# Optimization experiments

Hardware: AMD Instinct MI355X
Metric: run time of the kernel (lower is better)

The kernel has to match this reference:

```python
import math
import jax, jax.numpy as jnp
import numpy as np

L_MAX = 3
PADDED = (1, 1, 2, 3)            # padded_l_list
K_MAX_L = (128, 96, 64, 32)      # channel bounds per l
FEATS = (32, 32, 32, 32)         # k_max_l[l] - k_max_l[l+1]
N_ATOMS = 20000
N_EDGES = 80000
N_RADIAL = 32
HIDDEN = 128
EPS = 1e-6


def setup_inputs() -> dict:
    key = jax.random.key(0)
    ks = jax.random.split(key, 40)
    it = iter(range(40))
    nk = lambda: ks[next(it)]
    inp = {}
    inp['rb'] = jax.random.normal(nk(), (L_MAX + 1, N_EDGES, N_RADIAL), jnp.float32)
    for l in range(L_MAX + 1):
        inp[f'sh{l}'] = jax.random.normal(nk(), (N_EDGES, 2 * l + 1), jnp.float32)
    for l in range(L_MAX + 1):
        P = PADDED[l]
        inp[f'f{l}'] = jax.random.normal(nk(), (N_ATOMS, P + 1, P + 1, FEATS[l]), jnp.float32)
    for P in (1, 2, 3):
        n = (P + 1) ** 2
        inp[f'U{P}'] = jax.random.normal(nk(), (n, n), jnp.float32) / math.sqrt(n)
    inp['gammas'] = jnp.ones((L_MAX + 1, 32), jnp.float32)
    inp['Win'] = jax.random.normal(nk(), (L_MAX + 1, 32, 32), jnp.float32) / math.sqrt(32.0)
    inp['Wout'] = jax.random.normal(nk(), (L_MAX + 1, 32, 32), jnp.float32) / math.sqrt(32.0)
    inp['A'] = jax.random.normal(nk(), (L_MAX + 1, N_RADIAL, HIDDEN), jnp.float32) / math.sqrt(float(N_RADIAL))
    for l in range(L_MAX + 1):
        inp[f'B{l}'] = jax.random.normal(nk(), (HIDDEN, K_MAX_L[l]), jnp.float32) / math.sqrt(float(HIDDEN))
    inp['msg_scale'] = jnp.float32(0.5)
    inp['centers'] = jax.random.randint(nk(), (N_EDGES,), 0, N_ATOMS)
    inp['neighbors'] = jax.random.randint(nk(), (N_EDGES,), 0, N_ATOMS)
    return inp


def _forward(rb, shs, feats, Us, gammas, Win, Wout, A, Bs, msg_scale, centers, neighbors):
    n_atoms = feats[0].shape[0]
    # EquivariantRMSNorm (norm over uncoupled i,j indices per channel) + linear_in
    h = []
    for l in range(L_MAX + 1):
        f = feats[l]
        rms = jnp.sqrt(jnp.mean(f * f, axis=(1, 2), keepdims=True) + EPS)
        fn = (f / rms) * gammas[l]
        h.append(jnp.einsum('nijf,fg->nijg', fn, Win[l]))
    # per-l radial MLP: [E, n_radial] -> silu -> [E, k_max_l[l]]
    rbm = [jax.nn.silu(rb[l] @ A[l]) @ Bs[l] for l in range(L_MAX + 1)]
    # vector expansion [E, 2l+1, k_max_l[l]]
    vexp = [shs[l][:, :, None] * rbm[l][:, None, :] for l in range(L_MAX + 1)]
    # split channels into per-l groups, uncouple via CG matrix U
    unc = []
    for l in range(L_MAX + 1):
        lower = K_MAX_L[l + 1] if l < L_MAX else 0
        upper = K_MAX_L[l]
        group = [vexp[lp][:, :, lower:upper] for lp in range(l + 1)]
        P = PADDED[l]
        if len(group) < P + 1:
            group.append(jnp.zeros((N_EDGES, 2 * P + 1, upper - lower), group[0].dtype))
        stacked = jnp.concatenate(group, axis=1)  # [E, (P+1)^2, feat]
        u = jnp.einsum('pq,eqf->epf', Us[P], stacked)
        unc.append(u.reshape(N_EDGES, P + 1, P + 1, upper - lower))
    # gather -> per-l tensor product -> scatter-add -> linear_out -> residual
    out = []
    for l in range(L_MAX + 1):
        P = PADDED[l]
        msg = jnp.einsum('eijf,ejkf->eikf', unc[l], h[l][neighbors]) / math.sqrt(P + 1.0)
        pooled = jnp.zeros((n_atoms,) + msg.shape[1:], msg.dtype).at[centers].add(msg) * msg_scale
        out.append(feats[l] + jnp.einsum('nijf,fg->nijg', pooled, Wout[l]))
    return tuple(out)


def reference(rb, sh0, sh1, sh2, sh3, f0, f1, f2, f3, U1, U2, U3, gammas, Win, Wout, A, B0, B1, B2, B3, msg_scale, centers, neighbors):
    return _forward(rb, [sh0, sh1, sh2, sh3], [f0, f1, f2, f3], {1: U1, 2: U2, 3: U3}, gammas, Win, Wout, A, [B0, B1, B2, B3], msg_scale, centers, neighbors)
```

## Files before the change

### kernel.cpp

```cpp
#include <hip/hip_runtime.h>
#include <cstdint>

#define NA 20000
#define NE 80000

typedef __attribute__((ext_vector_type(8))) short short8;
typedef __attribute__((ext_vector_type(4))) float f32x4;
typedef unsigned short ushort_t;

constexpr int HOFFc[4]   = {0, 2560000, 5120000, 10880000};
constexpr int RBMOFFc[4] = {0, 128, 224, 288};

__device__ __forceinline__ ushort_t f2bf(float x) {
    union { float f; unsigned u; } v; v.f = x;
    unsigned r = v.u + 0x7fffu + ((v.u >> 16) & 1u);
    return (ushort_t)(r >> 16);
}
__device__ __forceinline__ float bf2f(ushort_t u) {
    union { unsigned u; float f; } v; v.u = ((unsigned)u) << 16;
    return v.f;
}
__device__ __forceinline__ unsigned pack2(float a, float b) {
    return ((unsigned)f2bf(b) << 16) | (unsigned)f2bf(a);
}

__global__ __launch_bounds__(256)
void k_prep_w(const float* __restrict__ B0, const float* __restrict__ B1,
              const float* __restrict__ B2, const float* __restrict__ B3,
              const float* __restrict__ A, const float* __restrict__ Win,
              ushort_t* __restrict__ BT, ushort_t* __restrict__ ATb,
              ushort_t* __restrict__ WinTb)
{
    const int i = blockIdx.x * 256 + threadIdx.x;
    if (i < 40960) {
        const int n = i >> 7, k = i & 127;
        const float* src; int nl, N;
        if (n < 128)      { src = B0; nl = n;       N = 128; }
        else if (n < 224) { src = B1; nl = n - 128; N = 96;  }
        else if (n < 288) { src = B2; nl = n - 224; N = 64;  }
        else              { src = B3; nl = n - 288; N = 32;  }
        BT[i] = f2bf(src[k * N + nl]);
    } else if (i < 57344) {
        const int j2 = i - 40960;
        const int l = j2 >> 12, rem = j2 & 4095, jrow = rem >> 5, k = rem & 31;
        ATb[j2] = f2bf(A[l * 4096 + k * 128 + jrow]);
    } else if (i < 61440) {
        const int j3 = i - 57344;
        const int l = j3 >> 10, rem = j3 & 1023, g = rem >> 5, k = rem & 31;
        WinTb[j3] = f2bf(Win[l * 1024 + k * 32 + g]);
    }
}

template<int S, int AB>
__device__ __forceinline__ void norm_body(
    const float* __restrict__ fsel, const float* __restrict__ gammas, int l,
    const ushort_t* __restrict__ WinTb, ushort_t* __restrict__ hb,
    ushort_t* __restrict__ s_wt, float* __restrict__ s_scale)
{
    const int t = threadIdx.x;
    const int na0 = blockIdx.x * AB;

    if (t < 128) {
        reinterpret_cast<uint4*>(s_wt)[t] =
            reinterpret_cast<const uint4*>(WinTb + l * 1024)[t];
    }
    for (int i = t; i < AB * 32; i += 256) {
        const int a = i >> 5, c = i & 31;
        int aa = na0 + a; if (aa > NA - 1) aa = NA - 1;
        const float* fp = fsel + ((size_t)aa * S) * 32 + c;
        float ss = 0.f;
        #pragma unroll
        for (int s = 0; s < S; ++s) { const float v = fp[s * 32]; ss += v * v; }
        s_scale[i] = gammas[l * 32 + c] * rsqrtf(ss / (float)S + 1e-6f);
    }
    __syncthreads();

    const int w = t >> 6, lane = t & 63, l15 = lane & 15, lg = lane >> 4;
    const int row = w * 16 + l15;
    const bool rvalid = row < AB * S;
    const int rowc = rvalid ? row : 0;
    const int a = rowc / S, s = rowc % S;
    const int atom = na0 + a;
    const bool store_ok = rvalid && (atom < NA);
    const int atomc = (atom < NA) ? atom : (NA - 1);

    const float* fp = fsel + ((size_t)atomc * S + s) * 32 + lg * 8;
    const float4 x0 = *reinterpret_cast<const float4*>(fp);
    const float4 x1 = *reinterpret_cast<const float4*>(fp + 4);
    const float4 c0 = *reinterpret_cast<const float4*>(&s_scale[a * 32 + lg * 8]);
    const float4 c1 = *reinterpret_cast<const float4*>(&s_scale[a * 32 + lg * 8 + 4]);

    union { short8 v; unsigned u[4]; } bf;
    bf.u[0] = pack2(x0.x * c0.x, x0.y * c0.y);
    bf.u[1] = pack2(x0.z * c0.z, x0.w * c0.w);
    bf.u[2] = pack2(x1.x * c1.x, x1.y * c1.y);
    bf.u[3] = pack2(x1.z * c1.z, x1.w * c1.w);

    const short8 a0 = *reinterpret_cast<const short8*>(&s_wt[l15 * 32 + lg * 8]);
    const short8 a1 = *reinterpret_cast<const short8*>(&s_wt[(16 + l15) * 32 + lg * 8]);
    f32x4 d0 = __builtin_amdgcn_mfma_f32_16x16x32_bf16(a0, bf.v, (f32x4){0.f,0.f,0.f,0.f}, 0, 0, 0);
    f32x4 d1 = __builtin_amdgcn_mfma_f32_16x16x32_bf16(a1, bf.v, (f32x4){0.f,0.f,0.f,0.f}, 0, 0, 0);

    if (store_ok) {
        ushort_t* hp = hb + ((size_t)atomc * S + s) * 32;
        uint2 o0; o0.x = pack2(d0[0], d0[1]); o0.y = pack2(d0[2], d0[3]);
        uint2 o1; o1.x = pack2(d1[0], d1[1]); o1.y = pack2(d1[2], d1[3]);
        *reinterpret_cast<uint2*>(&hp[0  + 4 * lg]) = o0;
        *reinterpret_cast<uint2*>(&hp[16 + 4 * lg]) = o1;
    }
}

__global__ __launch_bounds__(256, 8)
void k_norm_mfma(const float* __restrict__ f0, const float* __restrict__ f1,
                 const float* __restrict__ f2, const float* __restrict__ f3,
                 const float* __restrict__ gammas, const ushort_t* __restrict__ WinTb,
                 ushort_t* __restrict__ h)
{
    __shared__ ushort_t s_wt[1024];
    __shared__ float s_scale[512];
    const int l = blockIdx.y;
    if (l == 0) {
        if (blockIdx.x >= 1250) return;
        norm_body<4, 16>(f0, gammas, 0, WinTb, h + HOFFc[0], s_wt, s_scale);
    } else if (l == 1) {
        if (blockIdx.x >= 1250) return;
        norm_body<4, 16>(f1, gammas, 1, WinTb, h + HOFFc[1], s_wt, s_scale);
    } else if (l == 2) {
        if (blockIdx.x >= 2858) return;
        norm_body<9, 7>(f2, gammas, 2, WinTb, h + HOFFc[2], s_wt, s_scale);
    } else {
        norm_body<16, 4>(f3, gammas, 3, WinTb, h + HOFFc[3], s_wt, s_scale);
    }
}

__global__ __launch_bounds__(256, 3)
void k_edgeA(const float* __restrict__ rb,
             const float* __restrict__ sh0, const float* __restrict__ sh1,
             const float* __restrict__ sh2, const float* __restrict__ sh3,
             const ushort_t* __restrict__ BT, const ushort_t* __restrict__ ATb,
             ushort_t* __restrict__ rbm, float* __restrict__ shq)
{
    __shared__ ushort_t s_h[8192];
    __shared__ ushort_t s_r2[16384];
    ushort_t* s_rbbf = s_r2;
    ushort_t* s_at   = s_r2 + 2048;
    ushort_t* s_bt   = s_r2;

    const int t  = threadIdx.x;
    const int e0 = blockIdx.x * 64;
    const int l  = blockIdx.y;
    const int w  = t >> 6, lane = t & 63;
    const int l15 = lane & 15, lg = lane >> 4;

    if (l == 0) {
        for (int i = t; i < 1024; i += 256) {
            const int q = i & 15, ge = e0 + (i >> 4);
            float v;
            if (q == 0)      v = sh0[ge];
            else if (q < 4)  v = sh1[ge * 3 + (q - 1)];
            else if (q < 9)  v = sh2[ge * 5 + (q - 4)];
            else             v = sh3[ge * 7 + (q - 9)];
            shq[(size_t)e0 * 16 + i] = v;
        }
    }

    const int Kl[4] = {128, 96, 64, 32};
    const int erow = w * 16 + l15;

    for (int i = t; i < 1024; i += 256) {
        const float2 v = *reinterpret_cast<const float2*>(
            &rb[(size_t)l * NE * 32 + (size_t)e0 * 32 + 2 * i]);
        *reinterpret_cast<unsigned*>(&s_rbbf[2 * i]) = pack2(v.x, v.y);
    }
    {
        const uint4* src = reinterpret_cast<const uint4*>(ATb + (size_t)l * 4096);
        for (int i = t; i < 512; i += 256) reinterpret_cast<uint4*>(s_at)[i] = src[i];
    }
    __syncthreads();

    const short8 rbf = *reinterpret_cast<const short8*>(&s_rbbf[erow * 32 + lg * 8]);
    #pragma unroll
    for (int jt = 0; jt < 8; ++jt) {
        const short8 af = *reinterpret_cast<const short8*>(&s_at[(jt * 16 + l15) * 32 + lg * 8]);
        f32x4 d = __builtin_amdgcn_mfma_f32_16x16x32_bf16(af, rbf, (f32x4){0.f,0.f,0.f,0.f}, 0, 0, 0);
        float s0 = d[0] / (1.f + __expf(-d[0]));
        float s1 = d[1] / (1.f + __expf(-d[1]));
        float s2 = d[2] / (1.f + __expf(-d[2]));
        float s3 = d[3] / (1.f + __expf(-d[3]));
        const int chunk = jt * 2 + (lg >> 1);
        const int base = erow * 128 + ((chunk ^ (erow & 7)) << 3) + (lg & 1) * 4;
        uint2 ov; ov.x = pack2(s0, s1); ov.y = pack2(s2, s3);
        *reinterpret_cast<uint2*>(&s_h[base]) = ov;
    }
    __syncthreads();

    const int K = Kl[l];
    for (int cch = t; cch < (K << 4); cch += 256) {
        const int n = cch >> 4, loc = cch & 15;
        const uint4 v = *reinterpret_cast<const uint4*>(&BT[(size_t)(RBMOFFc[l] + n) * 128 + loc * 8]);
        *reinterpret_cast<uint4*>(&s_bt[n * 128 + ((loc ^ (n & 7)) << 3)]) = v;
    }
    __syncthreads();

    const short8 hf0 = *reinterpret_cast<const short8*>(&s_h[erow * 128 + (((0 + lg) ^ (erow & 7)) << 3)]);
    const short8 hf1 = *reinterpret_cast<const short8*>(&s_h[erow * 128 + (((4 + lg) ^ (erow & 7)) << 3)]);
    const short8 hf2 = *reinterpret_cast<const short8*>(&s_h[erow * 128 + (((8 + lg) ^ (erow & 7)) << 3)]);
    const short8 hf3 = *reinterpret_cast<const short8*>(&s_h[erow * 128 + (((12 + lg) ^ (erow & 7)) << 3)]);

    const int ntn = K >> 4;
    for (int nt = 0; nt < ntn; ++nt) {
        const int n = nt * 16 + l15;
        f32x4 acc = {0.f, 0.f, 0.f, 0.f};
        #pragma unroll
        for (int ks = 0; ks < 4; ++ks) {
            const short8 af = *reinterpret_cast<const short8*>(
                &s_bt[n * 128 + (((ks * 4 + lg) ^ (n & 7)) << 3)]);
            const short8 hfk = (ks == 0) ? hf0 : (ks == 1) ? hf1 : (ks == 2) ? hf2 : hf3;
            acc = __builtin_amdgcn_mfma_f32_16x16x32_bf16(af, hfk, acc, 0, 0, 0);
        }
        uint2 ov;
        ov.x = pack2(acc[0], acc[1]);
        ov.y = pack2(acc[2], acc[3]);
        *reinterpret_cast<uint2*>(&rbm[(size_t)(e0 + erow) * 320 + RBMOFFc[l] + nt * 16 + 4 * lg]) = ov;
    }
}

__global__ __launch_bounds__(256)
void k_hist(const int* __restrict__ centers, int* __restrict__ counts)
{
    const int e = blockIdx.x * 256 + threadIdx.x;
    if (e < NE) atomicAdd(&counts[centers[e]], 1);
}

__global__ __launch_bounds__(1024)
void k_scan(const int* __restrict__ counts, int* __restrict__ offsets)
{
    __shared__ int s_sum[1024];
    const int t = threadIdx.x;
    const int CH = 20;
    const int base = t * CH;
    int n = NA - base; n = n < 0 ? 0 : (n > CH ? CH : n);

    int tot = 0;
    for (int i = 0; i < n; i++) tot += counts[base + i];
    s_sum[t] = tot;
    __syncthreads();
    for (int off = 1; off < 1024; off <<= 1) {
        int v = (t >= off) ? s_sum[t - off] : 0;
        __syncthreads();
        s_sum[t] += v;
        __syncthreads();
    }
    int run = s_sum[t] - tot;
    for (int i = 0; i < n; i++) { offsets[base + i] = run; run += counts[base + i]; }
    if (t == 0) offsets[NA] = NE;
}

__global__ __launch_bounds__(256)
void k_fill(const int* __restrict__ centers, const int* __restrict__ offsets,
            int* __restrict__ cursor, int* __restrict__ elist)
{
    const int e = blockIdx.x * 256 + threadIdx.x;
    if (e < NE) {
        const int ctr = centers[e];
        const int pos = offsets[ctr] + atomicAdd(&cursor[ctr], 1);
        elist[pos] = e;
    }
}

template<int P1, int ASTART, int ACNT>
__device__ __forceinline__ void tp_step(float* __restrict__ acc,
                                        const float* __restrict__ lg,
                                        const ushort_t* __restrict__ lh,
                                        const float* __restrict__ rv, int c)
{
    float un[ACNT];
    #pragma unroll
    for (int pi = 0; pi < ACNT; ++pi) {
        const int p = ASTART + pi;
        float a = 0.f;
        #pragma unroll
        for (int lp = 0; lp < P1; ++lp) a += lg[p * 4 + lp] * rv[lp];
        un[pi] = a;
    }
    #pragma unroll
    for (int ii = 0; ii < ACNT / P1; ++ii) {
        #pragma unroll
        for (int k = 0; k < P1; ++k) {
            float m = 0.f;
            #pragma unroll
            for (int j = 0; j < P1; ++j) m += un[ii * P1 + j] * bf2f(lh[(j * P1 + k) * 32 + c]);
            acc[ii * P1 + k] += m;
        }
    }
}

template<int P1, int LOWER>
__global__ __launch_bounds__(256, 6)
void k_pool_big(const float* __restrict__ Up, float uscale,
                const float* __restrict__ WoutL, const float* __restrict__ msp,
                const float* __restrict__ shq, const ushort_t* __restrict__ rbm,
                const ushort_t* __restrict__ hL, const float* __restrict__ fL,
                float* __restrict__ outL,
                const int* __restrict__ offsets, const int* __restrict__ elist,
                const int* __restrict__ neighbors)
{
    constexpr int S       = P1 * P1;
    constexpr int ACNT0   = (P1 == 4) ? 8 : 6;
    constexpr int ACNT1   = (P1 == 4) ? 8 : 3;
    constexpr int ASTART1 = ACNT0;
    constexpr int NV      = (S * 32) / 8;

    __shared__ float    s_U[S * S];
    __shared__ float    s_w[1024];
    __shared__ ushort_t s_hbuf[4][2][S * 32];
    __shared__ float    s_gbuf[4][2][64];

    const int t = threadIdx.x;
    for (int i = t; i < S * S; i += 256) s_U[i] = Up[i] * uscale;
    for (int i = t; i < 1024; i += 256) s_w[i] = WoutL[i];
    __syncthreads();

    const int w = t >> 6, lane = t & 63, c = lane & 31, half = lane >> 5;
    const int n = blockIdx.x * 4 + w;
    const float ms = *msp;
    const int beg = offsets[n], end = offsets[n + 1];

    const int gp = lane >> 2, glp = lane & 3;
    const int qlo = (glp == 0) ? 0 : (glp == 1) ? 1 : (glp == 2) ? 4 : 9;
    const int qhi = (glp == 0) ? 1 : (glp == 1) ? 4 : (glp == 2) ? 9 : 16;
    const bool gvalid = (gp < S) && (glp < P1);

    float acc[ACNT0];
    #pragma unroll
    for (int x = 0; x < ACNT0; ++x) acc[x] = 0.f;

    ushort_t* lhA = s_hbuf[w][0];
    ushort_t* lhB = s_hbuf[w][1];
    float*    lgA = s_gbuf[w][0];
    float*    lgB = s_gbuf[w][1];

    for (int slot = beg; slot < end; slot += 2) {
        const bool haveB = (slot + 1) < end;
        const int eA = elist[slot];
        const int eB = elist[haveB ? slot + 1 : slot];
        const int nbrA = neighbors[eA];
        const int nbrB = neighbors[eB];

        uint4 vA = {}, vB = {};
        const uint4* hpA = reinterpret_cast<const uint4*>(hL + (size_t)nbrA * (S * 32));
        const uint4* hpB = reinterpret_cast<const uint4*>(hL + (size_t)nbrB * (S * 32));
        if (lane < NV) { vA = hpA[lane]; vB = hpB[lane]; }

        const ushort_t* rrA = rbm + (size_t)eA * 320 + LOWER + c;
        const ushort_t* rrB = rbm + (size_t)eB * 320 + LOWER + c;
        float rvA[4], rvB[4];
        #pragma unroll
        for (int lp = 0; lp < P1; ++lp) { rvA[lp] = bf2f(rrA[RBMOFFc[lp]]); rvB[lp] = bf2f(rrB[RBMOFFc[lp]]); }

        const float* sqA = shq + (size_t)eA * 16;
        const float* sqB = shq + (size_t)eB * 16;
        float gA = 0.f, gB = 0.f;
        if (gvalid) {
            for (int q = qlo; q < qhi; ++q) {
                const float u = s_U[gp * S + q];
                gA += u * sqA[q];
                gB += u * sqB[q];
            }
        }

        if (lane < NV) {
            reinterpret_cast<uint4*>(lhA)[lane] = vA;
            reinterpret_cast<uint4*>(lhB)[lane] = vB;
        }
        lgA[lane] = gA;
        lgB[lane] = gB;

        asm volatile("s_waitcnt lgkmcnt(0)" ::: "memory");

        if (half == 0) tp_step<P1, 0,       ACNT0>(acc, lgA, lhA, rvA, c);
        else           tp_step<P1, ASTART1, ACNT1>(acc, lgA, lhA, rvA, c);
        if (haveB) {
            if (half == 0) tp_step<P1, 0,       ACNT0>(acc, lgB, lhB, rvB, c);
            else           tp_step<P1, ASTART1, ACNT1>(acc, lgB, lhB, rvB, c);
        }
    }

    float* accStage = reinterpret_cast<float*>(s_hbuf[w]);
    if (half == 0) {
        #pragma unroll
        for (int x = 0; x < ACNT0; ++x) accStage[x * 32 + c] = acc[x];
    } else {
        #pragma unroll
        for (int x = 0; x < ACNT1; ++x) accStage[(ASTART1 + x) * 32 + c] = acc[x];
    }
    asm volatile("s_waitcnt lgkmcnt(0)" ::: "memory");

    const float* fp = fL + (size_t)n * (S * 32);
    float* op = outL + (size_t)n * (S * 32);
    for (int s = half; s < S; s += 2) {
        float o = 0.f;
        #pragma unroll
        for (int f = 0; f < 32; f++) o += accStage[s * 32 + f] * s_w[f * 32 + c];
        op[s * 32 + c] = fp[s * 32 + c] + ms * o;
    }
}

__global__ __launch_bounds__(256, 4)
void k_pool_01(const float* __restrict__ U1, const float* __restrict__ Wout,
               const float* __restrict__ msp, const float* __restrict__ shq,
               const ushort_t* __restrict__ rbm, const ushort_t* __restrict__ h,
               const float* __restrict__ f0, const float* __restrict__ f1,
               float* __restrict__ out,
               const int* __restrict__ offsets, const int* __restrict__ elist,
               const int* __restrict__ neighbors)
{
    __shared__ float s_U[16];
    __shared__ float s_w[2048];
    __shared__ float s_acc[4][2][128];

    const int t = threadIdx.x;
    if (t < 16) s_U[t] = U1[t] * 0.70710678118654752f;
    for (int i = t; i < 2048; i += 256) s_w[i] = Wout[i];
    __syncthreads();

    const int w = t >> 6, lane = t & 63, c = lane & 31, half = lane >> 5;
    const int n = blockIdx.x * 4 + w;
    const float ms = *msp;
    const int beg = offsets[n], end = offsets[n + 1];
    const ushort_t* h0 = h;
    const ushort_t* h1 = h + 2560000;

    float acc0[4] = {0.f, 0.f, 0.f, 0.f};
    float acc1[4] = {0.f, 0.f, 0.f, 0.f};

    const int nit = (end - beg + 1) >> 1;
    for (int it = 0; it < nit; ++it) {
        const int slot = beg + it * 2 + half;
        const bool valid = slot < end;
        const int e   = elist[valid ? slot : beg];
        const int nbr = neighbors[e];
        const float fac = valid ? 1.f : 0.f;

        const ushort_t* rrow = rbm + (size_t)e * 320;
        const float rv0  = fac * bf2f(rrow[96 + c]);
        const float rv1a = fac * bf2f(rrow[64 + c]);
        const float rv1b = fac * bf2f(rrow[192 + c]);
        const float* sqp = shq + (size_t)e * 16;
        const float sq0 = sqp[0], sq1 = sqp[1], sq2 = sqp[2], sq3 = sqp[3];

        float hn0[4], hn1[4];
        const ushort_t* hp0 = h0 + (size_t)nbr * 128 + c;
        const ushort_t* hp1 = h1 + (size_t)nbr * 128 + c;
        #pragma unroll
        for (int p = 0; p < 4; ++p) { hn0[p] = bf2f(hp0[p * 32]); hn1[p] = bf2f(hp1[p * 32]); }

        const float st0 = sq0 * rv0;
        float st1[4];
        st1[0] = sq0 * rv1a; st1[1] = sq1 * rv1b; st1[2] = sq2 * rv1b; st1[3] = sq3 * rv1b;

        float unc0[4], unc1[4];
        #pragma unroll
        for (int p = 0; p < 4; ++p) {
            unc0[p] = s_U[p * 4] * st0;
            float a = 0.f;
            #pragma unroll
            for (int q = 0; q < 4; ++q) a += s_U[p * 4 + q] * st1[q];
            unc1[p] = a;
        }
        #pragma unroll
        for (int i = 0; i < 2; ++i) {
            #pragma unroll
            for (int k = 0; k < 2; ++k) {
                float m0 = 0.f, m1 = 0.f;
                #pragma unroll
                for (int j = 0; j < 2; ++j) {
                    m0 += unc0[i * 2 + j] * hn0[j * 2 + k];
                    m1 += unc1[i * 2 + j] * hn1[j * 2 + k];
                }
                acc0[i * 2 + k] += m0;
                acc1[i * 2 + k] += m1;
            }
        }
    }

    #pragma unroll
    for (int s = 0; s < 4; s++) { acc0[s] += __shfl_xor(acc0[s], 32); acc1[s] += __shfl_xor(acc1[s], 32); }
    #pragma unroll
    for (int s = 0; s < 4; s++) if ((s & 1) == half) {
        s_acc[w][0][s * 32 + c] = acc0[s];
        s_acc[w][1][s * 32 + c] = acc1[s];
    }
    __syncthreads();

    const float* fp0 = f0 + (size_t)n * 128;
    const float* fp1 = f1 + (size_t)n * 128;
    float* op0 = out + (size_t)n * 128;
    float* op1 = out + 2560000 + (size_t)n * 128;
    for (int s = half; s < 4; s += 2) {
        float o0 = 0.f, o1 = 0.f;
        #pragma unroll
        for (int f = 0; f < 32; f++) {
            o0 += s_acc[w][0][s * 32 + f] * s_w[f * 32 + c];
            o1 += s_acc[w][1][s * 32 + f] * s_w[1024 + f * 32 + c];
        }
        op0[s * 32 + c] = fp0[s * 32 + c] + ms * o0;
        op1[s * 32 + c] = fp1[s * 32 + c] + ms * o1;
    }
}

extern "C" void kernel_launch(void* const* d_in, const int* in_sizes, int n_in,
                              void* d_out, int out_size, void* d_ws, size_t ws_size,
                              hipStream_t stream)
{
    (void)in_sizes; (void)n_in; (void)out_size;

    const float* rb     = (const float*)d_in[0];
    const float* sh0    = (const float*)d_in[1];
    const float* sh1    = (const float*)d_in[2];
    const float* sh2    = (const float*)d_in[3];
    const float* sh3    = (const float*)d_in[4];
    const float* f0     = (const float*)d_in[5];
    const float* f1     = (const float*)d_in[6];
    const float* f2     = (const float*)d_in[7];
    const float* f3     = (const float*)d_in[8];
    const float* U1     = (const float*)d_in[9];
    const float* U2     = (const float*)d_in[10];
    const float* U3     = (const float*)d_in[11];
    const float* gammas = (const float*)d_in[12];
    const float* Win    = (const float*)d_in[13];
    const float* Wout   = (const float*)d_in[14];
    const float* A      = (const float*)d_in[15];
    const float* B0     = (const float*)d_in[16];
    const float* B1     = (const float*)d_in[17];
    const float* B2     = (const float*)d_in[18];
    const float* B3     = (const float*)d_in[19];
    const float* msp    = (const float*)d_in[20];
    const int* centers   = (const int*)d_in[21];
    const int* neighbors = (const int*)d_in[22];

    const size_t OFF_RBM = 42240000;
    const size_t OFF_SHQ = 93440000;
    const size_t OFF_BT  = 98560000;
    const size_t OFF_AT  = 98641920;
    const size_t OFF_WT  = 98674688;
    const size_t OFF_INT = 98682880;
    const size_t needed  = OFF_INT + (size_t)140001 * 4;
    if (ws_size < needed) return;

    ushort_t* h_bf  = (ushort_t*)d_ws;
    ushort_t* rbm   = (ushort_t*)((char*)d_ws + OFF_RBM);
    float*    shq   = (float*)((char*)d_ws + OFF_SHQ);
    ushort_t* BT    = (ushort_t*)((char*)d_ws + OFF_BT);
    ushort_t* ATb   = (ushort_t*)((char*)d_ws + OFF_AT);
    ushort_t* WinTb = (ushort_t*)((char*)d_ws + OFF_WT);
    int* ibase   = (int*)((char*)d_ws + OFF_INT);
    int* offsets = ibase;
    int* counts  = ibase + 20001;
    int* cursor  = ibase + 40001;
    int* elist   = ibase + 60001;

    hipMemsetAsync(counts, 0, (size_t)40000 * sizeof(int), stream);

    k_hist<<<313, 256, 0, stream>>>(centers, counts);
    k_scan<<<1, 1024, 0, stream>>>(counts, offsets);
    k_fill<<<313, 256, 0, stream>>>(centers, offsets, cursor, elist);
    k_prep_w<<<240, 256, 0, stream>>>(B0, B1, B2, B3, A, Win, BT, ATb, WinTb);

    dim3 gN(5000, 4);
    k_norm_mfma<<<gN, 256, 0, stream>>>(f0, f1, f2, f3, gammas, WinTb, h_bf);
    dim3 gE(1250, 4);
    k_edgeA<<<gE, 256, 0, stream>>>(rb, sh0, sh1, sh2, sh3, BT, ATb, rbm, shq);

    float* out = (float*)d_out;
    k_pool_01<<<5000, 256, 0, stream>>>(U1, Wout, msp, shq, rbm, h_bf, f0, f1, out,
                                        offsets, elist, neighbors);
    k_pool_big<3, 32><<<5000, 256, 0, stream>>>(U2, 0.57735026918962576f, Wout + 2048, msp,
                                                shq, rbm, h_bf + HOFFc[2], f2, out + HOFFc[2],
                                                offsets, elist, neighbors);
    k_pool_big<4, 0><<<5000, 256, 0, stream>>>(U3, 0.5f, Wout + 3072, msp,
                                               shq, rbm, h_bf + HOFFc[3], f3, out + HOFFc[3],
                                               offsets, elist, neighbors);
}
```

Baseline: 306.8 us.

## Merge three pooling kernels into one launch and fuse histogram with weight prep

```diff
diff --git a/kernel.cpp b/kernel.cpp
--- a/kernel.cpp
+++ b/kernel.cpp
@@ -25,13 +25,20 @@
 }
 
 __global__ __launch_bounds__(256)
-void k_prep_w(const float* __restrict__ B0, const float* __restrict__ B1,
-              const float* __restrict__ B2, const float* __restrict__ B3,
-              const float* __restrict__ A, const float* __restrict__ Win,
-              ushort_t* __restrict__ BT, ushort_t* __restrict__ ATb,
-              ushort_t* __restrict__ WinTb)
-{
-    const int i = blockIdx.x * 256 + threadIdx.x;
+void k_hist_prep(const int* __restrict__ centers, int* __restrict__ counts,
+                 const float* __restrict__ B0, const float* __restrict__ B1,
+                 const float* __restrict__ B2, const float* __restrict__ B3,
+                 const float* __restrict__ A, const float* __restrict__ Win,
+                 ushort_t* __restrict__ BT, ushort_t* __restrict__ ATb,
+                 ushort_t* __restrict__ WinTb)
+{
+    const int b = blockIdx.x;
+    if (b < 313) {
+        const int e = b * 256 + threadIdx.x;
+        if (e < NE) atomicAdd(&counts[centers[e]], 1);
+        return;
+    }
+    const int i = (b - 313) * 256 + threadIdx.x;
     if (i < 40960) {
         const int n = i >> 7, k = i & 127;
         const float* src; int nl, N;
@@ -225,13 +232,6 @@
     }
 }
 
-__global__ __launch_bounds__(256)
-void k_hist(const int* __restrict__ centers, int* __restrict__ counts)
-{
-    const int e = blockIdx.x * 256 + threadIdx.x;
-    if (e < NE) atomicAdd(&counts[centers[e]], 1);
-}
-
 __global__ __launch_bounds__(1024)
 void k_scan(const int* __restrict__ counts, int* __restrict__ offsets)
 {
@@ -296,14 +296,14 @@
 }
 
 template<int P1, int LOWER>
-__global__ __launch_bounds__(256, 6)
-void k_pool_big(const float* __restrict__ Up, float uscale,
-                const float* __restrict__ WoutL, const float* __restrict__ msp,
-                const float* __restrict__ shq, const ushort_t* __restrict__ rbm,
-                const ushort_t* __restrict__ hL, const float* __restrict__ fL,
-                float* __restrict__ outL,
-                const int* __restrict__ offsets, const int* __restrict__ elist,
-                const int* __restrict__ neighbors)
+__device__ __forceinline__ void pool_big_body(
+    const float* __restrict__ Up, float uscale,
+    const float* __restrict__ WoutL, const float* __restrict__ msp,
+    const float* __restrict__ shq, const ushort_t* __restrict__ rbm,
+    const ushort_t* __restrict__ hL, const float* __restrict__ fL,
+    float* __restrict__ outL,
+    const int* __restrict__ offsets, const int* __restrict__ elist,
+    const int* __restrict__ neighbors, float* __restrict__ sm)
 {
     constexpr int S       = P1 * P1;
     constexpr int ACNT0   = (P1 == 4) ? 8 : 6;
@@ -311,10 +311,12 @@
     constexpr int ASTART1 = ACNT0;
     constexpr int NV      = (S * 32) / 8;
 
-    __shared__ float    s_U[S * S];
-    __shared__ float    s_w[1024];
-    __shared__ ushort_t s_hbuf[4][2][S * 32];
-    __shared__ float    s_gbuf[4][2][64];
+    float*    s_U    = sm;
+    float*    s_w    = sm + 256;
+    ushort_t* s_hbuf = reinterpret_cast<ushort_t*>(sm + 256 + 1024);
+    float*    s_gbuf = sm + 256 + 1024 + 64 * S;
+
+    s_gbuf = sm + 256 + 1024 + 128 * S;
 
     const int t = threadIdx.x;
     for (int i = t; i < S * S; i += 256) s_U[i] = Up[i] * uscale;
@@ -335,10 +337,10 @@
     #pragma unroll
     for (int x = 0; x < ACNT0; ++x) acc[x] = 0.f;
 
-    ushort_t* lhA = s_hbuf[w][0];
-    ushort_t* lhB = s_hbuf[w][1];
-    float*    lgA = s_gbuf[w][0];
-    float*    lgB = s_gbuf[w][1];
+    ushort_t* lhA = s_hbuf + w * 2 * (S * 32);
+    ushort_t* lhB = lhA + S * 32;
+    float*    lgA = s_gbuf + w * 128;
+    float*    lgB = lgA + 64;
 
     for (int slot = beg; slot < end; slot += 2) {
         const bool haveB = (slot + 1) < end;
@@ -386,7 +388,7 @@
         }
     }
 
-    float* accStage = reinterpret_cast<float*>(s_hbuf[w]);
+    float* accStage = reinterpret_cast<float*>(lhA);
     if (half == 0) {
         #pragma unroll
         for (int x = 0; x < ACNT0; ++x) accStage[x * 32 + c] = acc[x];
@@ -406,18 +408,18 @@
     }
 }
 
-__global__ __launch_bounds__(256, 4)
-void k_pool_01(const float* __restrict__ U1, const float* __restrict__ Wout,
-               const float* __restrict__ msp, const float* __restrict__ shq,
-               const ushort_t* __restrict__ rbm, const ushort_t* __restrict__ h,
-               const float* __restrict__ f0, const float* __restrict__ f1,
-               float* __restrict__ out,
-               const int* __restrict__ offsets, const int* __restrict__ elist,
-               const int* __restrict__ neighbors)
-{
-    __shared__ float s_U[16];
-    __shared__ float s_w[2048];
-    __shared__ float s_acc[4][2][128];
+__device__ __forceinline__ void pool_01_body(
+    const float* __restrict__ U1, const float* __restrict__ Wout,
+    const float* __restrict__ msp, const float* __restrict__ shq,
+    const ushort_t* __restrict__ rbm, const ushort_t* __restrict__ h,
+    const float* __restrict__ f0, const float* __restrict__ f1,
+    float* __restrict__ out,
+    const int* __restrict__ offsets, const int* __restrict__ elist,
+    const int* __restrict__ neighbors, float* __restrict__ sm)
+{
+    float* s_U   = sm;
+    float* s_w   = sm + 16;
+    float* s_acc = sm + 16 + 2048;
 
     const int t = threadIdx.x;
     if (t < 16) s_U[t] = U1[t] * 0.70710678118654752f;
@@ -488,8 +490,8 @@
     for (int s = 0; s < 4; s++) { acc0[s] += __shfl_xor(acc0[s], 32); acc1[s] += __shfl_xor(acc1[s], 32); }
     #pragma unroll
     for (int s = 0; s < 4; s++) if ((s & 1) == half) {
-        s_acc[w][0][s * 32 + c] = acc0[s];
-        s_acc[w][1][s * 32 + c] = acc1[s];
+        s_acc[(w * 2 + 0) * 128 + s * 32 + c] = acc0[s];
+        s_acc[(w * 2 + 1) * 128 + s * 32 + c] = acc1[s];
     }
     __syncthreads();
 
@@ -501,11 +503,38 @@
         float o0 = 0.f, o1 = 0.f;
         #pragma unroll
         for (int f = 0; f < 32; f++) {
-            o0 += s_acc[w][0][s * 32 + f] * s_w[f * 32 + c];
-            o1 += s_acc[w][1][s * 32 + f] * s_w[1024 + f * 32 + c];
+            o0 += s_acc[(w * 2 + 0) * 128 + s * 32 + f] * s_w[f * 32 + c];
+            o1 += s_acc[(w * 2 + 1) * 128 + s * 32 + f] * s_w[1024 + f * 32 + c];
         }
         op0[s * 32 + c] = fp0[s * 32 + c] + ms * o0;
         op1[s * 32 + c] = fp1[s * 32 + c] + ms * o1;
+    }
+}
+
+__global__ __launch_bounds__(256, 6)
+void k_pools(const float* __restrict__ U1, const float* __restrict__ U2,
+             const float* __restrict__ U3, const float* __restrict__ Wout,
+             const float* __restrict__ msp, const float* __restrict__ shq,
+             const ushort_t* __restrict__ rbm, const ushort_t* __restrict__ h,
+             const float* __restrict__ f0, const float* __restrict__ f1,
+             const float* __restrict__ f2, const float* __restrict__ f3,
+             float* __restrict__ out,
+             const int* __restrict__ offsets, const int* __restrict__ elist,
+             const int* __restrict__ neighbors)
+{
+    __shared__ float sm[3840];
+    const int which = blockIdx.y;
+    if (which == 0) {
+        pool_big_body<4, 0>(U3, 0.5f, Wout + 3072, msp, shq, rbm,
+                            h + HOFFc[3], f3, out + HOFFc[3],
+                            offsets, elist, neighbors, sm);
+    } else if (which == 1) {
+        pool_big_body<3, 32>(U2, 0.57735026918962576f, Wout + 2048, msp, shq, rbm,
+                             h + HOFFc[2], f2, out + HOFFc[2],
+                             offsets, elist, neighbors, sm);
+    } else {
+        pool_01_body(U1, Wout, msp, shq, rbm, h, f0, f1, out,
+                     offsets, elist, neighbors, sm);
     }
 }
 
@@ -562,23 +591,18 @@
 
     hipMemsetAsync(counts, 0, (size_t)40000 * sizeof(int), stream);
 
-    k_hist<<<313, 256, 0, stream>>>(centers, counts);
+    k_hist_prep<<<553, 256, 0, stream>>>(centers, counts, B0, B1, B2, B3, A, Win,
+                                         BT, ATb, WinTb);
     k_scan<<<1, 1024, 0, stream>>>(counts, offsets);
     k_fill<<<313, 256, 0, stream>>>(centers, offsets, cursor, elist);
-    k_prep_w<<<240, 256, 0, stream>>>(B0, B1, B2, B3, A, Win, BT, ATb, WinTb);
 
     dim3 gN(5000, 4);
     k_norm_mfma<<<gN, 256, 0, stream>>>(f0, f1, f2, f3, gammas, WinTb, h_bf);
     dim3 gE(1250, 4);
     k_edgeA<<<gE, 256, 0, stream>>>(rb, sh0, sh1, sh2, sh3, BT, ATb, rbm, shq);
 
-    float* out = (float*)d_out;
-    k_pool_01<<<5000, 256, 0, stream>>>(U1, Wout, msp, shq, rbm, h_bf, f0, f1, out,
-                                        offsets, elist, neighbors);
-    k_pool_big<3, 32><<<5000, 256, 0, stream>>>(U2, 0.57735026918962576f, Wout + 2048, msp,
-                                                shq, rbm, h_bf + HOFFc[2], f2, out + HOFFc[2],
-                                                offsets, elist, neighbors);
-    k_pool_big<4, 0><<<5000, 256, 0, stream>>>(U3, 0.5f, Wout + 3072, msp,
-                                               shq, rbm, h_bf + HOFFc[3], f3, out + HOFFc[3],
-                                               offsets, elist, neighbors);
-}
+    dim3 gP(5000, 3);
+    k_pools<<<gP, 256, 0, stream>>>(U1, U2, U3, Wout, msp, shq, rbm, h_bf,
+                                    f0, f1, f2, f3, (float*)d_out,
+                                    offsets, elist, neighbors);
+}
```

New measurement: 282.3 us. -8.0%, faster.
